# Kernel tuning notes

Hardware: AMD Instinct MI355X
Metric: run time of the kernel (lower is better)

The kernel has to match this reference:

```python
import jax, jax.numpy as jnp
import numpy as np
from jax import lax

B, L, DIN, DOUT, K = 8, 4096, 256, 256, 3


def _gates(x, W, b, k):
    # x: [B, L, Din] -> conv over time, channels-first like torch Conv1d
    xt = jnp.transpose(x, (0, 2, 1))  # [B, Din, L]
    pad = (k - 1) // 2
    g = lax.conv_general_dilated(xt, W, window_strides=(1,), padding=[(pad, pad)],
                                 dimension_numbers=("NCH", "OIH", "NCH"))
    g = g + b[None, :, None]
    g = jnp.transpose(g, (0, 2, 1))  # [B, L, 3*Dout]
    f, o, z = jnp.split(g, 3, axis=-1)
    return jax.nn.sigmoid(f), jax.nn.sigmoid(o), jnp.tanh(z)


def _fo_pool(f, z, init_cell, reverse):
    # c_t = f_t * c_{t-1} + (1 - f_t) * z_t ; scan over time axis
    fT = jnp.transpose(f, (1, 0, 2))  # [L, B, D]
    zT = jnp.transpose(z, (1, 0, 2))

    def step(c, fz):
        ft, zt = fz
        c = ft * c + (1.0 - ft) * zt
        return c, c

    _, cells = lax.scan(step, init_cell, (fT, zT), reverse=reverse)
    return jnp.transpose(cells, (1, 0, 2))  # [B, L, D]


def setup_inputs() -> dict:
    key = jax.random.key(0)
    k1, k2, k3, k4, k5, k6 = jax.random.split(key, 6)
    scale_in = 1.0 / np.sqrt(DIN * K)
    inp = {
        "input": jax.random.normal(k1, (B, L, DIN), dtype=jnp.float32),
        "lengths": jnp.full((B,), L, dtype=jnp.int64) if False else jax.random.randint(k2, (B,), 1, L + 1),
        "W_fwd": jax.random.uniform(k3, (3 * DOUT, DIN, K), dtype=jnp.float32, minval=-scale_in, maxval=scale_in),
        "b_fwd": jax.random.uniform(k4, (3 * DOUT,), dtype=jnp.float32, minval=-scale_in, maxval=scale_in),
        "W_bwd": jax.random.uniform(k5, (3 * DOUT, DIN, K), dtype=jnp.float32, minval=-scale_in, maxval=scale_in),
        "b_bwd": jax.random.uniform(k6, (3 * DOUT,), dtype=jnp.float32, minval=-scale_in, maxval=scale_in),
    }
    return inp


def reference(input, lengths, W_fwd, b_fwd, W_bwd, b_bwd):
    init_cell = jnp.zeros((input.shape[0], DOUT), dtype=input.dtype)

    # forward direction
    f, o, z = _gates(input, W_fwd, b_fwd, K)
    cell = _fo_pool(f, z, init_cell, reverse=False)
    hidden = cell * o

    # backward direction
    fr, orr, zr = _gates(input, W_bwd, b_bwd, K)
    rcell = _fo_pool(fr, zr, init_cell, reverse=True)
    rhidden = rcell * orr

    output = jnp.concatenate([hidden, rhidden], axis=-1)  # [B, L, 2*Dout]
    last_h = jnp.concatenate([hidden[:, -1, :], rhidden[:, -1, :]], axis=-1)
    last_c = jnp.concatenate([cell[:, -1, :], rcell[:, -1, :]], axis=-1)
    return output, last_h, last_c
```

## Files before the change

kernel.cpp:

```cpp
#include <hip/hip_runtime.h>
#include <hip/hip_bf16.h>
#include <hip/hip_fp16.h>

#define B_     8
#define L_     4096
#define DIN    256
#define DOUT   256
#define NGATE  1536
#define KDIM   768
#define LP     (L_ + 2)
#define CHUNK  32
#define NCHUNK (L_ / CHUNK)

typedef short    short8  __attribute__((ext_vector_type(8)));
typedef __bf16   bf16x8  __attribute__((ext_vector_type(8)));
typedef float    floatx4 __attribute__((ext_vector_type(4)));
typedef _Float16 half4   __attribute__((ext_vector_type(4)));

__device__ __forceinline__ float fast_sigmoid(float x) {
    return __builtin_amdgcn_rcpf(1.f + __expf(-x));
}
__device__ __forceinline__ float fast_tanh(float x) {
    return 1.f - 2.f * __builtin_amdgcn_rcpf(1.f + __expf(2.f * x));
}
__device__ __forceinline__ unsigned short f2bf(float x) {
    unsigned u = __float_as_uint(x);
    u += 0x7FFF + ((u >> 16) & 1);
    return (unsigned short)(u >> 16);
}
__device__ __forceinline__ void gload16(const unsigned short* g, unsigned short* l) {
    __builtin_amdgcn_global_load_lds((const __attribute__((address_space(1))) void*)g,
                                     (__attribute__((address_space(3))) void*)l,
                                     16, 0, 0);
}

__device__ __forceinline__ int gate_noff(int n) {
    return (n >> 7) * 32768 + ((n >> 6) & 1) * 4096 + ((n >> 4) & 3) * 1024 + (n & 15) * 4;
}
__device__ __forceinline__ int gate_toff(int b, int t) {
    return (b * 16 + (t >> 8)) * 393216 + ((t >> 6) & 3) * 8192
         + ((t >> 4) & 3) * 256 + ((t >> 2) & 3) * 64;
}

#define NXB ((B_ * LP * 64 + 255) / 256)
#define NWB ((NGATE * KDIM + 255) / 256)
__global__ void prep_all(const float* __restrict__ x, unsigned short* __restrict__ Xp,
                         const float* __restrict__ Wf, const float* __restrict__ bf_,
                         const float* __restrict__ Wb, const float* __restrict__ bb,
                         unsigned short* __restrict__ Wc, float* __restrict__ bc) {
    if (blockIdx.x < NXB) {
        int idx = blockIdx.x * 256 + threadIdx.x;
        int row = idx >> 6;
        if (row >= B_ * LP) return;
        int c4 = (idx & 63) << 2;
        int b = row / LP, r = row - b * LP;
        float4 v = make_float4(0.f, 0.f, 0.f, 0.f);
        if (r >= 1 && r <= L_) {
            v = *(const float4*)(x + ((size_t)(b * L_ + (r - 1))) * DIN + c4);
        }
        ushort4 o = make_ushort4(f2bf(v.x), f2bf(v.y), f2bf(v.z), f2bf(v.w));
        *(ushort4*)(Xp + (size_t)row * DIN + c4) = o;
    } else {
        int gid = (blockIdx.x - NXB) * 256 + threadIdx.x;
        if (gid < NGATE) {
            bc[gid] = (gid < 768) ? bf_[gid] : bb[gid - 768];
        }
        if (gid >= NGATE * KDIM) return;
        int n = gid / KDIM, k = gid - n * KDIM;
        int s = k >> 8, ic = k & 255;
        const float* W = (n < 768) ? Wf : Wb;
        int oc = (n < 768) ? n : n - 768;
        float v = W[(size_t)oc * KDIM + ic * 3 + s];
        Wc[(size_t)n * KDIM + k] = f2bf(v);
    }
}

__launch_bounds__(512)
__global__ void gemm_gates(const unsigned short* __restrict__ Xp,
                           const unsigned short* __restrict__ Wc,
                           const float* __restrict__ bc,
                           _Float16* __restrict__ gates) {
    __shared__ unsigned short As[256 * 64];
    __shared__ unsigned short Bs[128 * 64];
    const int tid  = threadIdx.x;
    const int lane = tid & 63, wave = tid >> 6;
    const int quad = lane >> 4, l16 = lane & 15;
    const int wr = wave >> 1, wcl = wave & 1;

    int flat = blockIdx.x;
    int xcd  = flat & 7;
    int slot = flat >> 3;
    int bm   = xcd * 16 + slot / 12;
    int nblk = slot % 12;
    const int b  = bm >> 4;
    const int t0 = (bm & 15) << 8;
    const int n0 = nblk << 7;
    const unsigned short* Ab = Xp + (size_t)b * LP * DIN;

    int rowA[4], cgA[4], rowB[2], cgB[2];
#pragma unroll
    for (int j = 0; j < 4; j++) {
        int G = (wave * 4 + j) * 64 + lane;
        rowA[j] = G >> 3;
        cgA[j]  = ((G & 7) ^ (rowA[j] & 7)) * 8;
    }
#pragma unroll
    for (int j = 0; j < 2; j++) {
        int G = (wave * 2 + j) * 64 + lane;
        rowB[j] = G >> 3;
        cgB[j]  = ((G & 7) ^ (rowB[j] & 7)) * 8;
    }

    floatx4 acc[4][4];
#pragma unroll
    for (int i = 0; i < 4; i++)
#pragma unroll
        for (int j = 0; j < 4; j++) acc[i][j] = (floatx4)0.f;

    for (int k0 = 0; k0 < KDIM; k0 += 64) {
        const int sh = k0 >> 8;
        const int c0 = k0 & 255;
#pragma unroll
        for (int j = 0; j < 4; j++)
            gload16(Ab + (size_t)(t0 + rowA[j] + sh) * DIN + c0 + cgA[j],
                    &As[(wave * 4 + j) * 512]);
#pragma unroll
        for (int j = 0; j < 2; j++)
            gload16(Wc + (size_t)(n0 + rowB[j]) * KDIM + k0 + cgB[j],
                    &Bs[(wave * 2 + j) * 512]);
        __syncthreads();
#pragma unroll
        for (int kk = 0; kk < 2; kk++) {
            const int g0 = kk * 4 + quad;
            short8 af[4], bfr[4];
#pragma unroll
            for (int mi = 0; mi < 4; mi++) {
                int row = wr * 64 + mi * 16 + l16;
                af[mi] = *(const short8*)&As[row * 64 + ((g0 ^ (row & 7)) << 3)];
            }
#pragma unroll
            for (int ni = 0; ni < 4; ni++) {
                int row = wcl * 64 + ni * 16 + l16;
                bfr[ni] = *(const short8*)&Bs[row * 64 + ((g0 ^ (row & 7)) << 3)];
            }
#pragma unroll
            for (int mi = 0; mi < 4; mi++)
#pragma unroll
                for (int ni = 0; ni < 4; ni++)
                    acc[mi][ni] = __builtin_amdgcn_mfma_f32_16x16x32_bf16(
                        __builtin_bit_cast(bf16x8, af[mi]),
                        __builtin_bit_cast(bf16x8, bfr[ni]),
                        acc[mi][ni], 0, 0, 0);
        }
        __syncthreads();
    }

    const int cls = ((n0 + wcl * 64) >> 8) % 3;
    _Float16* gb = gates + ((size_t)(bm * 12 + nblk) * 8 + wave) * 4096 + lane * 4;
#pragma unroll
    for (int ni = 0; ni < 4; ni++) {
        float bias = bc[n0 + wcl * 64 + ni * 16 + l16];
#pragma unroll
        for (int mi = 0; mi < 4; mi++) {
            half4 hv;
#pragma unroll
            for (int rr = 0; rr < 4; rr++) {
                float v = acc[mi][ni][rr] + bias;
                v = (cls == 2) ? fast_tanh(v) : fast_sigmoid(v);
                hv[rr] = (_Float16)v;
            }
            *(half4*)(gb + (ni * 4 + mi) * 256) = hv;
        }
    }
}

__global__ void scan_chunks(const _Float16* __restrict__ gates,
                            float2* __restrict__ PW) {
    const int d = threadIdx.x;
    const int s = blockIdx.x, b = blockIdx.y, dir = blockIdx.z;
    const int onf = gate_noff(dir * 768 + d);
    const int onz = gate_noff(dir * 768 + 512 + d);
    float P = 1.f, W = 0.f;
    if (dir == 0) {
#pragma unroll
        for (int gi = 0; gi < 8; gi++) {
            int t = s * CHUNK + gi * 4;
            int ot = gate_toff(b, t);
            half4 f4 = *(const half4*)(gates + ot + onf);
            half4 z4 = *(const half4*)(gates + ot + onz);
#pragma unroll
            for (int u = 0; u < 4; u++) {
                float f = (float)f4[u], z = (float)z4[u];
                W = f * W + (1.f - f) * z;
                P *= f;
            }
        }
    } else {
#pragma unroll
        for (int gi = 7; gi >= 0; gi--) {
            int t = s * CHUNK + gi * 4;
            int ot = gate_toff(b, t);
            half4 f4 = *(const half4*)(gates + ot + onf);
            half4 z4 = *(const half4*)(gates + ot + onz);
#pragma unroll
            for (int u = 3; u >= 0; u--) {
                float f = (float)f4[u], z = (float)z4[u];
                W = f * W + (1.f - f) * z;
                P *= f;
            }
        }
    }
    PW[(((size_t)(dir * 8 + b)) * NCHUNK + s) * 256 + d] = make_float2(P, W);
}

__global__ void scan_seq(const float2* __restrict__ PW, float* __restrict__ C0) {
    const int c = threadIdx.x;
    const int dir = blockIdx.x >> 3, b = blockIdx.x & 7;
    const size_t base = ((size_t)(dir * 8 + b)) * NCHUNK * 256 + c;
    float cc = 0.f;
    if (dir == 0) {
#pragma unroll 16
        for (int s = 0; s < NCHUNK; s++) {
            float2 pw = PW[base + (size_t)s * 256];
            C0[base + (size_t)s * 256] = cc;
            cc = pw.x * cc + pw.y;
        }
    } else {
#pragma unroll 16
        for (int s = NCHUNK - 1; s >= 0; s--) {
            float2 pw = PW[base + (size_t)s * 256];
            C0[base + (size_t)s * 256] = cc;
            cc = pw.x * cc + pw.y;
        }
    }
}

__global__ void scan_final(const _Float16* __restrict__ gates,
                           const float* __restrict__ C0,
                           float* __restrict__ out) {
    __shared__ float hbuf[4][256];
    const int d = threadIdx.x;
    const int s = blockIdx.x, b = blockIdx.y, dir = blockIdx.z;
    const int onf = gate_noff(dir * 768 + d);
    const int ono = gate_noff(dir * 768 + 256 + d);
    const int onz = gate_noff(dir * 768 + 512 + d);
    float c = C0[(((size_t)(dir * 8 + b)) * NCHUNK + s) * 256 + d];
    float* ob = out + (size_t)(b * L_) * (2 * DOUT) + dir * DOUT;
    float* lasth = out + (size_t)B_ * L_ * (2 * DOUT);
    float* lastc = lasth + B_ * (2 * DOUT);
    const int tl = d >> 6, cl = (d & 63) * 4;

    for (int gg = 0; gg < 8; gg++) {
        int gi = (dir == 0) ? gg : 7 - gg;
        int t = s * CHUNK + gi * 4;
        int ot = gate_toff(b, t);
        half4 f4 = *(const half4*)(gates + ot + onf);
        half4 o4 = *(const half4*)(gates + ot + ono);
        half4 z4 = *(const half4*)(gates + ot + onz);
        float h[4];
        if (dir == 0) {
#pragma unroll
            for (int u = 0; u < 4; u++) {
                float f = (float)f4[u], z = (float)z4[u];
                c = f * c + (1.f - f) * z;
                h[u] = c * (float)o4[u];
            }
            if (s == NCHUNK - 1 && gi == 7) {
                lasth[b * 2 * DOUT + d] = h[3];
                lastc[b * 2 * DOUT + d] = c;
            }
        } else {
#pragma unroll
            for (int u = 3; u >= 0; u--) {
                float f = (float)f4[u], z = (float)z4[u];
                c = f * c + (1.f - f) * z;
                h[u] = c * (float)o4[u];
                if (u == 3 && s == NCHUNK - 1 && gi == 7) {
                    lasth[b * 2 * DOUT + DOUT + d] = h[3];
                    lastc[b * 2 * DOUT + DOUT + d] = c;
                }
            }
        }
        hbuf[0][d] = h[0];
        hbuf[1][d] = h[1];
        hbuf[2][d] = h[2];
        hbuf[3][d] = h[3];
        __syncthreads();
        *(float4*)&ob[(size_t)(t + tl) * (2 * DOUT) + cl] = *(float4*)&hbuf[tl][cl];
        __syncthreads();
    }
}

extern "C" void kernel_launch(void* const* d_in, const int* in_sizes, int n_in,
                              void* d_out, int out_size, void* d_ws, size_t ws_size,
                              hipStream_t stream) {
    const float* x   = (const float*)d_in[0];
    const float* Wf  = (const float*)d_in[2];
    const float* bfv = (const float*)d_in[3];
    const float* Wb  = (const float*)d_in[4];
    const float* bbv = (const float*)d_in[5];

    char* ws = (char*)d_ws;
    unsigned short* Xp    = (unsigned short*)(ws);
    unsigned short* Wc    = (unsigned short*)(ws + 16785408);
    float*          bc    = (float*)(ws + 19144704);
    _Float16*       gates = (_Float16*)(ws + 19150848);
    float2*         PW    = (float2*)(ws);
    float*          C0    = (float*)(ws + 4194304);
    float*          out   = (float*)d_out;

    prep_all<<<NXB + NWB, 256, 0, stream>>>(x, Xp, Wf, bfv, Wb, bbv, Wc, bc);
    gemm_gates<<<1536, 512, 0, stream>>>(Xp, Wc, bc, gates);
    scan_chunks<<<dim3(NCHUNK, B_, 2), 256, 0, stream>>>(gates, PW);
    scan_seq<<<16, 256, 0, stream>>>(PW, C0);
    scan_final<<<dim3(NCHUNK, B_, 2), 256, 0, stream>>>(gates, C0, out);
}
```

Before: 218.9 us.

## Enlarge GEMM tile to 256x256 with double-buffered LDS and phased prefetch

Rewrites the gate GEMM to use 256x256 output tiles per block, halving the grid. Each block double-buffers A and B in LDS and splits every k-step into four quadrant phases that issue the next step's global-to-LDS loads while MFMAs run, using raw barriers, waitcnt and setprio. The gate tensor layout and the scan index helpers change to match the new tile shape. This aims to raise MFMA arithmetic intensity and hide load latency, at the cost of 128KB of LDS per block and more register pressure, which may lower occupancy.

```diff
diff --git a/kernel.cpp b/kernel.cpp
--- a/kernel.cpp
+++ b/kernel.cpp
@@ -11,6 +11,7 @@
 #define LP     (L_ + 2)
 #define CHUNK  32
 #define NCHUNK (L_ / CHUNK)
+#define NKSTEP (KDIM / 64)
 
 typedef short    short8  __attribute__((ext_vector_type(8)));
 typedef __bf16   bf16x8  __attribute__((ext_vector_type(8)));
@@ -35,11 +36,12 @@
 }
 
 __device__ __forceinline__ int gate_noff(int n) {
-    return (n >> 7) * 32768 + ((n >> 6) & 1) * 4096 + ((n >> 4) & 3) * 1024 + (n & 15) * 4;
+    return (n >> 8) * 65536 + ((n >> 5) & 3) * 8192
+         + (((n >> 7) & 1) * 2 + ((n >> 4) & 1)) * 2048 + (n & 15) * 4;
 }
 __device__ __forceinline__ int gate_toff(int b, int t) {
-    return (b * 16 + (t >> 8)) * 393216 + ((t >> 6) & 3) * 8192
-         + ((t >> 4) & 3) * 256 + ((t >> 2) & 3) * 64;
+    return (b * 16 + (t >> 8)) * 393216 + ((t >> 6) & 1) * 32768
+         + (((t >> 7) & 1) * 4 + ((t >> 4) & 3)) * 256 + ((t >> 2) & 3) * 64;
 }
 
 #define NXB ((B_ * LP * 64 + 255) / 256)
@@ -75,101 +77,138 @@
     }
 }
 
-__launch_bounds__(512)
+__launch_bounds__(512, 2)
 __global__ void gemm_gates(const unsigned short* __restrict__ Xp,
                            const unsigned short* __restrict__ Wc,
                            const float* __restrict__ bc,
                            _Float16* __restrict__ gates) {
-    __shared__ unsigned short As[256 * 64];
-    __shared__ unsigned short Bs[128 * 64];
+    __shared__ alignas(16) unsigned short As[2][16384];
+    __shared__ alignas(16) unsigned short Bs[2][16384];
     const int tid  = threadIdx.x;
-    const int lane = tid & 63, wave = tid >> 6;
+    const int lane = tid & 63, w = tid >> 6;
     const int quad = lane >> 4, l16 = lane & 15;
-    const int wr = wave >> 1, wcl = wave & 1;
+    const int wr = w >> 2, wcl = w & 3;
 
     int flat = blockIdx.x;
     int xcd  = flat & 7;
     int slot = flat >> 3;
-    int bm   = xcd * 16 + slot / 12;
-    int nblk = slot % 12;
+    int bm   = xcd * 16 + slot / 6;
+    int nblk = slot % 6;
     const int b  = bm >> 4;
     const int t0 = (bm & 15) << 8;
-    const int n0 = nblk << 7;
+    const int n0 = nblk << 8;
     const unsigned short* Ab = Xp + (size_t)b * LP * DIN;
 
-    int rowA[4], cgA[4], rowB[2], cgB[2];
-#pragma unroll
-    for (int j = 0; j < 4; j++) {
-        int G = (wave * 4 + j) * 64 + lane;
-        rowA[j] = G >> 3;
-        cgA[j]  = ((G & 7) ^ (rowA[j] & 7)) * 8;
-    }
+    int rS[2], cgS[2];
 #pragma unroll
     for (int j = 0; j < 2; j++) {
-        int G = (wave * 2 + j) * 64 + lane;
-        rowB[j] = G >> 3;
-        cgB[j]  = ((G & 7) ^ (rowB[j] & 7)) * 8;
-    }
-
-    floatx4 acc[4][4];
-#pragma unroll
-    for (int i = 0; i < 4; i++)
+        int G = (j * 8 + w) * 64 + lane;
+        rS[j]  = G >> 3;
+        cgS[j] = ((G & 7) ^ (rS[j] & 7)) * 8;
+    }
+
+    floatx4 acc[8][4];
+#pragma unroll
+    for (int i = 0; i < 8; i++)
 #pragma unroll
         for (int j = 0; j < 4; j++) acc[i][j] = (floatx4)0.f;
 
-    for (int k0 = 0; k0 < KDIM; k0 += 64) {
-        const int sh = k0 >> 8;
-        const int c0 = k0 & 255;
-#pragma unroll
-        for (int j = 0; j < 4; j++)
-            gload16(Ab + (size_t)(t0 + rowA[j] + sh) * DIN + c0 + cgA[j],
-                    &As[(wave * 4 + j) * 512]);
-#pragma unroll
-        for (int j = 0; j < 2; j++)
-            gload16(Wc + (size_t)(n0 + rowB[j]) * KDIM + k0 + cgB[j],
-                    &Bs[(wave * 2 + j) * 512]);
-        __syncthreads();
-#pragma unroll
-        for (int kk = 0; kk < 2; kk++) {
-            const int g0 = kk * 4 + quad;
-            short8 af[4], bfr[4];
-#pragma unroll
-            for (int mi = 0; mi < 4; mi++) {
-                int row = wr * 64 + mi * 16 + l16;
-                af[mi] = *(const short8*)&As[row * 64 + ((g0 ^ (row & 7)) << 3)];
-            }
-#pragma unroll
-            for (int ni = 0; ni < 4; ni++) {
-                int row = wcl * 64 + ni * 16 + l16;
-                bfr[ni] = *(const short8*)&Bs[row * 64 + ((g0 ^ (row & 7)) << 3)];
-            }
-#pragma unroll
-            for (int mi = 0; mi < 4; mi++)
-#pragma unroll
-                for (int ni = 0; ni < 4; ni++)
-                    acc[mi][ni] = __builtin_amdgcn_mfma_f32_16x16x32_bf16(
-                        __builtin_bit_cast(bf16x8, af[mi]),
-                        __builtin_bit_cast(bf16x8, bfr[ni]),
-                        acc[mi][ni], 0, 0, 0);
-        }
-        __syncthreads();
-    }
-
-    const int cls = ((n0 + wcl * 64) >> 8) % 3;
-    _Float16* gb = gates + ((size_t)(bm * 12 + nblk) * 8 + wave) * 4096 + lane * 4;
-#pragma unroll
-    for (int ni = 0; ni < 4; ni++) {
-        float bias = bc[n0 + wcl * 64 + ni * 16 + l16];
-#pragma unroll
-        for (int mi = 0; mi < 4; mi++) {
+#define STAGE_A(ks, mh, cb) do {                                               \
+    const int sh_ = (ks) >> 2, c0_ = ((ks) & 3) * 64;                          \
+    _Pragma("unroll")                                                          \
+    for (int j_ = 0; j_ < 2; ++j_)                                             \
+        gload16(Ab + (size_t)(t0 + (mh) * 128 + rS[j_] + sh_) * DIN + c0_ + cgS[j_], \
+                &As[cb][(mh) * 8192 + (j_ * 8 + w) * 512]);                    \
+} while (0)
+
+#define STAGE_B(ks, nh, cb) do {                                               \
+    const int k0_ = (ks) * 64;                                                 \
+    _Pragma("unroll")                                                          \
+    for (int j_ = 0; j_ < 2; ++j_)                                             \
+        gload16(Wc + (size_t)(n0 + (nh) * 128 + rS[j_]) * KDIM + k0_ + cgS[j_], \
+                &Bs[cb][(nh) * 8192 + (j_ * 8 + w) * 512]);                    \
+} while (0)
+
+#define PHASE(mh, nh, cb, STG) do {                                            \
+    short8 afr[4][2], bfr[2][2];                                               \
+    _Pragma("unroll")                                                          \
+    for (int m_ = 0; m_ < 4; ++m_) {                                           \
+        const int R = (mh) * 128 + wr * 64 + m_ * 16 + l16;                    \
+        const int rx = R & 7;                                                  \
+        afr[m_][0] = *(const short8*)&As[cb][R * 64 + ((quad ^ rx) << 3)];     \
+        afr[m_][1] = *(const short8*)&As[cb][R * 64 + (((4 + quad) ^ rx) << 3)]; \
+    }                                                                          \
+    _Pragma("unroll")                                                          \
+    for (int n_ = 0; n_ < 2; ++n_) {                                           \
+        const int R = (nh) * 128 + wcl * 32 + n_ * 16 + l16;                   \
+        const int rx = R & 7;                                                  \
+        bfr[n_][0] = *(const short8*)&Bs[cb][R * 64 + ((quad ^ rx) << 3)];     \
+        bfr[n_][1] = *(const short8*)&Bs[cb][R * 64 + (((4 + quad) ^ rx) << 3)]; \
+    }                                                                          \
+    STG;                                                                       \
+    __builtin_amdgcn_s_barrier();                                              \
+    asm volatile("s_waitcnt lgkmcnt(0)" ::: "memory");                         \
+    __builtin_amdgcn_s_setprio(1);                                             \
+    _Pragma("unroll")                                                          \
+    for (int m_ = 0; m_ < 4; ++m_)                                             \
+    _Pragma("unroll")                                                          \
+    for (int n_ = 0; n_ < 2; ++n_) {                                           \
+        acc[(mh)*4 + m_][(nh)*2 + n_] = __builtin_amdgcn_mfma_f32_16x16x32_bf16( \
+            __builtin_bit_cast(bf16x8, afr[m_][0]),                            \
+            __builtin_bit_cast(bf16x8, bfr[n_][0]),                            \
+            acc[(mh)*4 + m_][(nh)*2 + n_], 0, 0, 0);                           \
+        acc[(mh)*4 + m_][(nh)*2 + n_] = __builtin_amdgcn_mfma_f32_16x16x32_bf16( \
+            __builtin_bit_cast(bf16x8, afr[m_][1]),                            \
+            __builtin_bit_cast(bf16x8, bfr[n_][1]),                            \
+            acc[(mh)*4 + m_][(nh)*2 + n_], 0, 0, 0);                           \
+    }                                                                          \
+    __builtin_amdgcn_s_setprio(0);                                             \
+} while (0)
+
+#define WINDOW(kv, cb, nb) do {                                                \
+    const int k_ = (kv);                                                       \
+    PHASE(0, 0, cb, { if (k_ + 1 < NKSTEP) STAGE_A(k_ + 1, 1, nb); });         \
+    __builtin_amdgcn_s_barrier();                                              \
+    PHASE(1, 0, cb, { if (k_ + 1 < NKSTEP) STAGE_B(k_ + 1, 1, nb); });         \
+    __builtin_amdgcn_s_barrier();                                              \
+    PHASE(0, 1, cb, { if (k_ + 2 < NKSTEP) STAGE_B(k_ + 2, 0, cb); });         \
+    __builtin_amdgcn_s_barrier();                                              \
+    PHASE(1, 1, cb, { if (k_ + 2 < NKSTEP) STAGE_A(k_ + 2, 0, cb); });         \
+    if (k_ + 2 < NKSTEP) { asm volatile("s_waitcnt vmcnt(4)" ::: "memory"); }  \
+    else                 { asm volatile("s_waitcnt vmcnt(0)" ::: "memory"); }  \
+    __builtin_amdgcn_s_barrier();                                              \
+} while (0)
+
+    STAGE_A(0, 0, 0); STAGE_B(0, 0, 0); STAGE_A(0, 1, 0); STAGE_B(0, 1, 0);
+    STAGE_A(1, 0, 1); STAGE_B(1, 0, 1);
+    asm volatile("s_waitcnt vmcnt(4)" ::: "memory");
+    __builtin_amdgcn_s_barrier();
+
+    for (int kp = 0; kp < NKSTEP / 2; ++kp) {
+        WINDOW(2 * kp,     0, 1);
+        WINDOW(2 * kp + 1, 1, 0);
+    }
+
+#undef WINDOW
+#undef PHASE
+#undef STAGE_B
+#undef STAGE_A
+
+    const int cls = nblk % 3;
+    _Float16* gb = gates + ((size_t)((bm * 6 + nblk) * 8 + w)) * 8192 + lane * 4;
+#pragma unroll
+    for (int ni = 0; ni < 4; ++ni) {
+        const float bias = bc[n0 + (ni >> 1) * 128 + wcl * 32 + (ni & 1) * 16 + l16];
+#pragma unroll
+        for (int mi = 0; mi < 8; ++mi) {
             half4 hv;
 #pragma unroll
-            for (int rr = 0; rr < 4; rr++) {
+            for (int rr = 0; rr < 4; ++rr) {
                 float v = acc[mi][ni][rr] + bias;
                 v = (cls == 2) ? fast_tanh(v) : fast_sigmoid(v);
                 hv[rr] = (_Float16)v;
             }
-            *(half4*)(gb + (ni * 4 + mi) * 256) = hv;
+            *(half4*)(gb + (ni * 8 + mi) * 256) = hv;
         }
     }
 }
@@ -310,7 +349,7 @@
     float*          out   = (float*)d_out;
 
     prep_all<<<NXB + NWB, 256, 0, stream>>>(x, Xp, Wf, bfv, Wb, bbv, Wc, bc);
-    gemm_gates<<<1536, 512, 0, stream>>>(Xp, Wc, bc, gates);
+    gemm_gates<<<768, 512, 0, stream>>>(Xp, Wc, bc, gates);
     scan_chunks<<<dim3(NCHUNK, B_, 2), 256, 0, stream>>>(gates, PW);
     scan_seq<<<16, 256, 0, stream>>>(PW, C0);
     scan_final<<<dim3(NCHUNK, B_, 2), 256, 0, stream>>>(gates, C0, out);
```

Result: slower. 235.8 us (+7.7%).
